# Performance work log

Hardware: AMD Instinct MI355X
Metric: run time of the kernel (lower is better)

## Reference

```python
import jax, jax.numpy as jnp
import numpy as np

N_ATOM, N_QUERY, KNN = 100000, 20000, 32
E = N_QUERY * KNN
HID, EDGE_F, HEADS = 128, 16, 8
D_HEAD = HID // HEADS
LN_EPS = 1e-5


def setup_inputs() -> dict:
    key = jax.random.key(0)
    ks = jax.random.split(key, 16)
    s = 1.0 / np.sqrt(HID)
    src = jax.random.randint(ks[0], (E,), 0, N_ATOM)
    dst = jnp.repeat(jnp.arange(N_QUERY), KNN)  # each query has KNN incoming edges
    return {
        "h_atom": jax.random.normal(ks[1], (N_ATOM, HID), jnp.float32),
        "h_query": jax.random.normal(ks[2], (N_QUERY, HID), jnp.float32),
        "edge_attr": jax.random.uniform(ks[3], (E, EDGE_F), jnp.float32),
        "W_q": jax.random.normal(ks[4], (HID, HID), jnp.float32) * s,
        "W_k": jax.random.normal(ks[5], (HID, HID), jnp.float32) * s,
        "W_v": jax.random.normal(ks[6], (HID, HID), jnp.float32) * s,
        "W_rbf": jax.random.normal(ks[7], (HEADS, EDGE_F), jnp.float32) * (1.0 / np.sqrt(EDGE_F)),
        "W1": jax.random.normal(ks[8], (HID, 2 * HID), jnp.float32) * (1.0 / np.sqrt(2 * HID)),
        "b1": jnp.zeros((HID,), jnp.float32),
        "W2": jax.random.normal(ks[9], (HID, HID), jnp.float32) * s,
        "b2": jnp.zeros((HID,), jnp.float32),
        "ln_gamma": jnp.ones((HID,), jnp.float32),
        "ln_beta": jnp.zeros((HID,), jnp.float32),
        "edge_index": jnp.stack([src, dst]),
        "n_query": N_QUERY,
    }


def reference(h_atom, h_query, edge_attr, W_q, W_k, W_v, W_rbf, W1, b1, W2, b2,
              ln_gamma, ln_beta, edge_index, n_query):
    src, dst = edge_index[0], edge_index[1]
    En = src.shape[0]
    # gather + project, per-edge multi-head Q/K/V  [E, H, d]
    Q = (h_query[dst] @ W_q.T).reshape(En, HEADS, D_HEAD)
    K = (h_atom[src] @ W_k.T).reshape(En, HEADS, D_HEAD)
    V = (h_atom[src] @ W_v.T).reshape(En, HEADS, D_HEAD)
    scores = jnp.einsum("ehd,ehd->eh", Q, K) / np.sqrt(D_HEAD) + edge_attr @ W_rbf.T  # [E,H]
    # segment softmax over edges sharing the same dst query, per head
    seg_max = jax.lax.stop_gradient(jax.ops.segment_max(scores, dst, num_segments=n_query))
    ex = jnp.exp(scores - seg_max[dst])
    denom = jax.ops.segment_sum(ex, dst, num_segments=n_query)
    alpha = ex / (denom[dst] + 1e-16)  # [E,H]
    # weighted scatter-add aggregation
    msgs = (alpha[:, :, None] * V).reshape(En, HID)
    agg = jax.ops.segment_sum(msgs, dst, num_segments=n_query)  # [Nq, HID]
    # update MLP + residual + LayerNorm
    z = jnp.concatenate([h_query, agg], axis=-1)
    delta = jax.nn.relu(z @ W1.T + b1) @ W2.T + b2
    y = h_query + delta
    mu = y.mean(-1, keepdims=True)
    var = y.var(-1, keepdims=True)
    return (y - mu) / jnp.sqrt(var + LN_EPS) * ln_gamma + ln_beta
```

## Files before the change

kernel.cpp:

```cpp
#include <hip/hip_runtime.h>
#include <hip/hip_bf16.h>
#include <math.h>

#define N_ATOM   100000
#define N_QUERY  20000
#define KNN      32
#define EDGES    (N_QUERY * KNN)

typedef __attribute__((ext_vector_type(8))) short  short8;
typedef __attribute__((ext_vector_type(4))) float  floatx4;
typedef __attribute__((ext_vector_type(2))) float  fx2;

static __device__ __forceinline__ unsigned short f2bf_bits(float f) {
  union { __hip_bfloat16 h; unsigned short u; } cv;
  cv.h = __float2bfloat16(f);
  return cv.u;
}
static __device__ __forceinline__ float bflo(unsigned int u) { return __uint_as_float(u << 16); }
static __device__ __forceinline__ float bfhi(unsigned int u) { return __uint_as_float(u & 0xffff0000u); }

__global__ void pack_all_kernel(const float* __restrict__ Wq, const float* __restrict__ Wk,
                                const float* __restrict__ Wv, const float* __restrict__ W1,
                                const float* __restrict__ W2,
                                const float* __restrict__ edge_attr, const float* __restrict__ Wrbf,
                                unsigned short* __restrict__ WKVp, unsigned short* __restrict__ WQp,
                                unsigned short* __restrict__ W1p,  unsigned short* __restrict__ W2p,
                                float* __restrict__ ED) {
  int tid = blockIdx.x * blockDim.x + threadIdx.x;
  if (tid < 98304) {
    const float *Wa, *Wb; int nsplit, Kd, Nd; unsigned short* dst; float scale = 1.0f;
    int t = tid;
    if (t < 32768)      { Wa = Wk; Wb = Wv; nsplit = 128; Kd = 128; Nd = 256; dst = WKVp; }
    else if (t < 49152) { t -= 32768; Wa = Wq; Wb = Wq; nsplit = 128; Kd = 128; Nd = 128; dst = WQp; scale = 0.25f; }
    else if (t < 81920) { t -= 49152; Wa = W1; Wb = W1; nsplit = 128; Kd = 256; Nd = 128; dst = W1p; }
    else                { t -= 81920; Wa = W2; Wb = W2; nsplit = 128; Kd = 128; Nd = 128; dst = W2p; }
    int j    = t & 7;
    int lane = (t >> 3) & 63;
    int t2   = t >> 9;
    int NT   = Nd >> 4;
    int ntile = t2 % NT;
    int ktile = t2 / NT;
    int k = ktile * 32 + (lane >> 4) * 8 + j;
    int n = ntile * 16 + (lane & 15);
    float v = (n < nsplit) ? Wa[(size_t)n * Kd + k] : Wb[(size_t)(n - nsplit) * Kd + k];
    dst[t] = f2bf_bits(v * scale);
  } else {
    int e = tid - 98304;
    if (e >= EDGES) return;
    const float4* ea = (const float4*)(edge_attr + (size_t)e * 16);
    float4 x0 = ea[0], x1 = ea[1], x2 = ea[2], x3 = ea[3];
    float4 r0, r1;
#pragma unroll
    for (int h = 0; h < 8; h++) {
      const float4* wp = (const float4*)(Wrbf + h * 16);
      float4 w0 = wp[0], w1 = wp[1], w2 = wp[2], w3 = wp[3];
      float d = w0.x*x0.x + w0.y*x0.y + w0.z*x0.z + w0.w*x0.w
              + w1.x*x1.x + w1.y*x1.y + w1.z*x1.z + w1.w*x1.w
              + w2.x*x2.x + w2.y*x2.y + w2.z*x2.z + w2.w*x2.w
              + w3.x*x3.x + w3.y*x3.y + w3.z*x3.z + w3.w*x3.w;
      if (h < 4) ((float*)&r0)[h] = d; else ((float*)&r1)[h - 4] = d;
    }
    float4* dst = (float4*)(ED + (size_t)e * 8);
    dst[0] = r0; dst[1] = r1;
  }
}

__global__ __launch_bounds__(256, 2) void gemm_kvq(
    const float* __restrict__ h_atom, const float* __restrict__ h_query,
    const unsigned short* __restrict__ WKVp, const unsigned short* __restrict__ WQp,
    unsigned char* __restrict__ Kp8, unsigned char* __restrict__ Vp8,
    unsigned short* __restrict__ Qb) {
  constexpr int KB = (N_ATOM + 63) / 64;
  __shared__ unsigned short Wlds[32768];
  const int tid  = threadIdx.x;
  const int l    = tid & 63;
  const int w    = tid >> 6;
  const int quad = l >> 4;
  const int col0 = l & 15;

  if ((int)blockIdx.x < KB) {
    const int row0 = blockIdx.x * 64 + w * 16;
    const int grow = row0 + col0;
    int arow = grow < N_ATOM ? grow : N_ATOM - 1;

    const float* aptr = h_atom + (size_t)arow * 128 + quad * 8;
    floatx4 a[8];
#pragma unroll
    for (int k0 = 0; k0 < 4; k0++) {
      a[2 * k0]     = *(const floatx4*)(aptr + k0 * 32);
      a[2 * k0 + 1] = *(const floatx4*)(aptr + k0 * 32 + 4);
    }

    {
      const uint4* gsrc = (const uint4*)WKVp;
      uint4* ldst = (uint4*)Wlds;
#pragma unroll
      for (int it = 0; it < 16; it++)
        ldst[it * 256 + tid] = gsrc[it * 256 + tid];
    }

    short8 af[4];
#pragma unroll
    for (int k0 = 0; k0 < 4; k0++) {
      af[k0][0] = (short)f2bf_bits(a[2*k0][0]); af[k0][1] = (short)f2bf_bits(a[2*k0][1]);
      af[k0][2] = (short)f2bf_bits(a[2*k0][2]); af[k0][3] = (short)f2bf_bits(a[2*k0][3]);
      af[k0][4] = (short)f2bf_bits(a[2*k0+1][0]); af[k0][5] = (short)f2bf_bits(a[2*k0+1][1]);
      af[k0][6] = (short)f2bf_bits(a[2*k0+1][2]); af[k0][7] = (short)f2bf_bits(a[2*k0+1][3]);
    }
    __syncthreads();

    floatx4 acc[16];
#pragma unroll
    for (int i = 0; i < 16; i++) acc[i] = (floatx4){0.f, 0.f, 0.f, 0.f};
#pragma unroll
    for (int k0 = 0; k0 < 4; k0++) {
      const unsigned short* bbase = Wlds + k0 * 16 * 512 + l * 8;
#pragma unroll
      for (int nt = 0; nt < 16; nt++) {
        short8 bf = *(const short8*)(bbase + nt * 512);
        acc[nt] = __builtin_amdgcn_mfma_f32_16x16x32_bf16(bf, af[k0], acc[nt], 0, 0, 0);
      }
    }

    if (grow < N_ATOM) {
      unsigned char* kbase = Kp8 + (size_t)grow * 128 + quad * 4;
      unsigned char* vbase = Vp8 + (size_t)grow * 128 + quad * 4;
#pragma unroll
      for (int nt = 0; nt < 16; nt++) {
        int pk = __builtin_amdgcn_cvt_pk_fp8_f32(acc[nt][0], acc[nt][1], 0, false);
        pk     = __builtin_amdgcn_cvt_pk_fp8_f32(acc[nt][2], acc[nt][3], pk, true);
        if (nt < 8) *(int*)(kbase + nt * 16) = pk;
        else        *(int*)(vbase + (nt - 8) * 16) = pk;
      }
    }
  } else {
    const int row0 = ((int)blockIdx.x - KB) * 64 + w * 16;
    const int grow = row0 + col0;
    int arow = grow < N_QUERY ? grow : N_QUERY - 1;

    const float* aptr = h_query + (size_t)arow * 128 + quad * 8;
    floatx4 a[8];
#pragma unroll
    for (int k0 = 0; k0 < 4; k0++) {
      a[2 * k0]     = *(const floatx4*)(aptr + k0 * 32);
      a[2 * k0 + 1] = *(const floatx4*)(aptr + k0 * 32 + 4);
    }
    {
      const uint4* gsrc = (const uint4*)WQp;
      uint4* ldst = (uint4*)Wlds;
#pragma unroll
      for (int it = 0; it < 8; it++)
        ldst[it * 256 + tid] = gsrc[it * 256 + tid];
    }
    short8 af[4];
#pragma unroll
    for (int k0 = 0; k0 < 4; k0++) {
      af[k0][0] = (short)f2bf_bits(a[2*k0][0]); af[k0][1] = (short)f2bf_bits(a[2*k0][1]);
      af[k0][2] = (short)f2bf_bits(a[2*k0][2]); af[k0][3] = (short)f2bf_bits(a[2*k0][3]);
      af[k0][4] = (short)f2bf_bits(a[2*k0+1][0]); af[k0][5] = (short)f2bf_bits(a[2*k0+1][1]);
      af[k0][6] = (short)f2bf_bits(a[2*k0+1][2]); af[k0][7] = (short)f2bf_bits(a[2*k0+1][3]);
    }
    __syncthreads();

    floatx4 acc[8];
#pragma unroll
    for (int i = 0; i < 8; i++) acc[i] = (floatx4){0.f, 0.f, 0.f, 0.f};
#pragma unroll
    for (int k0 = 0; k0 < 4; k0++) {
      const unsigned short* bbase = Wlds + k0 * 8 * 512 + l * 8;
#pragma unroll
      for (int nt = 0; nt < 8; nt++) {
        short8 bf = *(const short8*)(bbase + nt * 512);
        acc[nt] = __builtin_amdgcn_mfma_f32_16x16x32_bf16(bf, af[k0], acc[nt], 0, 0, 0);
      }
    }

    if (grow < N_QUERY) {
#pragma unroll
      for (int nt = 0; nt < 8; nt++) {
        unsigned u0 = (unsigned)f2bf_bits(acc[nt][0]) | ((unsigned)f2bf_bits(acc[nt][1]) << 16);
        unsigned u1 = (unsigned)f2bf_bits(acc[nt][2]) | ((unsigned)f2bf_bits(acc[nt][3]) << 16);
        uint2 uu; uu.x = u0; uu.y = u1;
        *(uint2*)(Qb + (size_t)grow * 128 + nt * 16 + quad * 4) = uu;
      }
    }
  }
}

__global__ __launch_bounds__(256, 4) void attn_kernel(
    const unsigned short* __restrict__ Qb,
    const unsigned char* __restrict__ Kp8,
    const unsigned char* __restrict__ Vp8,
    const float* __restrict__ ED,
    const int* __restrict__ src,
    float* __restrict__ Agg) {
  const int l = threadIdx.x & 63;
  const int w = threadIdx.x >> 6;
  const int q = blockIdx.x * 4 + w;
  const int j = l >> 3;
  const int h = l & 7;
  const int e0 = q * KNN;

  int s0 = src[e0 +  0 + j];
  int s1 = src[e0 +  8 + j];
  int s2 = src[e0 + 16 + j];
  int s3 = src[e0 + 24 + j];

  const float* edp = ED + (size_t)e0 * 8 + l;
  float ed0 = edp[0];
  float ed1 = edp[64];
  float ed2 = edp[128];
  float ed3 = edp[192];

  const uint4* qp = (const uint4*)(Qb + (size_t)q * 128 + h * 16);
  uint4 qA = qp[0], qB = qp[1];

  uint4 kq0 = *(const uint4*)(Kp8 + (size_t)s0 * 128 + h * 16);
  uint4 kq1 = *(const uint4*)(Kp8 + (size_t)s1 * 128 + h * 16);
  uint4 kq2 = *(const uint4*)(Kp8 + (size_t)s2 * 128 + h * 16);
  uint4 kq3 = *(const uint4*)(Kp8 + (size_t)s3 * 128 + h * 16);
  uint4 vq0 = *(const uint4*)(Vp8 + (size_t)s0 * 128 + h * 16);
  uint4 vq1 = *(const uint4*)(Vp8 + (size_t)s1 * 128 + h * 16);
  uint4 vq2 = *(const uint4*)(Vp8 + (size_t)s2 * 128 + h * 16);
  uint4 vq3 = *(const uint4*)(Vp8 + (size_t)s3 * 128 + h * 16);

  float qd[16];
  qd[0]  = bflo(qA.x); qd[1]  = bfhi(qA.x); qd[2]  = bflo(qA.y); qd[3]  = bfhi(qA.y);
  qd[4]  = bflo(qA.z); qd[5]  = bfhi(qA.z); qd[6]  = bflo(qA.w); qd[7]  = bfhi(qA.w);
  qd[8]  = bflo(qB.x); qd[9]  = bfhi(qB.x); qd[10] = bflo(qB.y); qd[11] = bfhi(qB.y);
  qd[12] = bflo(qB.z); qd[13] = bfhi(qB.z); qd[14] = bflo(qB.w); qd[15] = bfhi(qB.w);

  float acc[16];
#pragma unroll
  for (int i = 0; i < 16; i++) acc[i] = 0.f;
  float lsum = 0.f;

  auto dopass = [&](const uint4& kq, const uint4& vq, float ed) {
    float kd = 0.f;
    {
      fx2 f0, f1;
      f0 = __builtin_amdgcn_cvt_pk_f32_fp8((int)kq.x, false);
      f1 = __builtin_amdgcn_cvt_pk_f32_fp8((int)kq.x, true);
      kd += qd[0] * f0[0] + qd[1] * f0[1] + qd[2] * f1[0] + qd[3] * f1[1];
      f0 = __builtin_amdgcn_cvt_pk_f32_fp8((int)kq.y, false);
      f1 = __builtin_amdgcn_cvt_pk_f32_fp8((int)kq.y, true);
      kd += qd[4] * f0[0] + qd[5] * f0[1] + qd[6] * f1[0] + qd[7] * f1[1];
      f0 = __builtin_amdgcn_cvt_pk_f32_fp8((int)kq.z, false);
      f1 = __builtin_amdgcn_cvt_pk_f32_fp8((int)kq.z, true);
      kd += qd[8] * f0[0] + qd[9] * f0[1] + qd[10] * f1[0] + qd[11] * f1[1];
      f0 = __builtin_amdgcn_cvt_pk_f32_fp8((int)kq.w, false);
      f1 = __builtin_amdgcn_cvt_pk_f32_fp8((int)kq.w, true);
      kd += qd[12] * f0[0] + qd[13] * f0[1] + qd[14] * f1[0] + qd[15] * f1[1];
    }
    float pe = __expf(kd + ed);
    lsum += pe;
    {
      fx2 g0, g1;
      g0 = __builtin_amdgcn_cvt_pk_f32_fp8((int)vq.x, false);
      g1 = __builtin_amdgcn_cvt_pk_f32_fp8((int)vq.x, true);
      acc[0] += pe * g0[0]; acc[1] += pe * g0[1]; acc[2] += pe * g1[0]; acc[3] += pe * g1[1];
      g0 = __builtin_amdgcn_cvt_pk_f32_fp8((int)vq.y, false);
      g1 = __builtin_amdgcn_cvt_pk_f32_fp8((int)vq.y, true);
      acc[4] += pe * g0[0]; acc[5] += pe * g0[1]; acc[6] += pe * g1[0]; acc[7] += pe * g1[1];
      g0 = __builtin_amdgcn_cvt_pk_f32_fp8((int)vq.z, false);
      g1 = __builtin_amdgcn_cvt_pk_f32_fp8((int)vq.z, true);
      acc[8] += pe * g0[0]; acc[9] += pe * g0[1]; acc[10] += pe * g1[0]; acc[11] += pe * g1[1];
      g0 = __builtin_amdgcn_cvt_pk_f32_fp8((int)vq.w, false);
      g1 = __builtin_amdgcn_cvt_pk_f32_fp8((int)vq.w, true);
      acc[12] += pe * g0[0]; acc[13] += pe * g0[1]; acc[14] += pe * g1[0]; acc[15] += pe * g1[1];
    }
  };
  dopass(kq0, vq0, ed0);
  dopass(kq1, vq1, ed1);
  dopass(kq2, vq2, ed2);
  dopass(kq3, vq3, ed3);

  lsum += __shfl_xor(lsum, 8, 64);
  lsum += __shfl_xor(lsum, 16, 64);
  lsum += __shfl_xor(lsum, 32, 64);

  float r8[8];
  const bool hiA = (l & 32) != 0;
#pragma unroll
  for (int i = 0; i < 8; i++) {
    float keep = hiA ? acc[i + 8] : acc[i];
    float send = hiA ? acc[i]     : acc[i + 8];
    r8[i] = keep + __shfl_xor(send, 32, 64);
  }
  float r4[4];
  const bool hiB = (l & 16) != 0;
#pragma unroll
  for (int i = 0; i < 4; i++) {
    float keep = hiB ? r8[i + 4] : r8[i];
    float send = hiB ? r8[i]     : r8[i + 4];
    r4[i] = keep + __shfl_xor(send, 16, 64);
  }
  float r2[2];
  const bool hiC = (l & 8) != 0;
#pragma unroll
  for (int i = 0; i < 2; i++) {
    float keep = hiC ? r4[i + 2] : r4[i];
    float send = hiC ? r4[i]     : r4[i + 2];
    r2[i] = keep + __shfl_xor(send, 8, 64);
  }
  float inv = 1.f / (lsum + 1e-16f);
  float2 o; o.x = r2[0] * inv; o.y = r2[1] * inv;
  *(float2*)(Agg + (size_t)q * 128 + h * 16 + 2 * j) = o;
}

__global__ __launch_bounds__(256, 1) void mlp_kernel(
    const float* __restrict__ h_query, const float* __restrict__ Agg,
    const unsigned short* __restrict__ W1p, const unsigned short* __restrict__ W2p,
    const float* __restrict__ b1, const float* __restrict__ b2,
    const float* __restrict__ gamma, const float* __restrict__ beta,
    float* __restrict__ out) {
  constexpr int M = N_QUERY;
  constexpr int STRIDE = 136;
  __shared__ unsigned short Wlds[16384];
  __shared__ unsigned short hid[64 * STRIDE];

  const int tid  = threadIdx.x;
  const int l    = tid & 63;
  const int w    = tid >> 6;
  const int quad = l >> 4;
  const int col0 = l & 15;
  const int row0 = blockIdx.x * 64 + w * 16;
  const int grow = row0 + col0;
  const int arow = grow < M ? grow : M - 1;

  const float* hp = h_query + (size_t)arow * 128 + quad * 8;
  const float* gp = Agg     + (size_t)arow * 128 + quad * 8;
  floatx4 a[16];
#pragma unroll
  for (int k0 = 0; k0 < 4; k0++) {
    a[2*k0]       = *(const floatx4*)(hp + k0 * 32);
    a[2*k0+1]     = *(const floatx4*)(hp + k0 * 32 + 4);
    a[8 + 2*k0]   = *(const floatx4*)(gp + k0 * 32);
    a[8 + 2*k0+1] = *(const floatx4*)(gp + k0 * 32 + 4);
  }

  {
    const uint4* gsrc = (const uint4*)W1p;
    uint4* ldst = (uint4*)Wlds;
#pragma unroll
    for (int it = 0; it < 8; it++) ldst[it * 256 + tid] = gsrc[it * 256 + tid];
  }

  short8 af[8];
#pragma unroll
  for (int t = 0; t < 8; t++) {
    af[t][0] = (short)f2bf_bits(a[2*t][0]);   af[t][1] = (short)f2bf_bits(a[2*t][1]);
    af[t][2] = (short)f2bf_bits(a[2*t][2]);   af[t][3] = (short)f2bf_bits(a[2*t][3]);
    af[t][4] = (short)f2bf_bits(a[2*t+1][0]); af[t][5] = (short)f2bf_bits(a[2*t+1][1]);
    af[t][6] = (short)f2bf_bits(a[2*t+1][2]); af[t][7] = (short)f2bf_bits(a[2*t+1][3]);
  }
  __syncthreads();

  floatx4 acc[8];
#pragma unroll
  for (int i = 0; i < 8; i++) acc[i] = (floatx4){0.f, 0.f, 0.f, 0.f};
#pragma unroll
  for (int kt = 0; kt < 4; kt++) {
    const unsigned short* bbase = Wlds + kt * 4096 + l * 8;
#pragma unroll
    for (int nt = 0; nt < 8; nt++) {
      short8 bf = *(const short8*)(bbase + nt * 512);
      acc[nt] = __builtin_amdgcn_mfma_f32_16x16x32_bf16(bf, af[kt], acc[nt], 0, 0, 0);
    }
  }
  __syncthreads();

  {
    const uint4* gsrc = (const uint4*)(W1p + 16384);
    uint4* ldst = (uint4*)Wlds;
#pragma unroll
    for (int it = 0; it < 8; it++) ldst[it * 256 + tid] = gsrc[it * 256 + tid];
  }
  __syncthreads();

#pragma unroll
  for (int kt = 0; kt < 4; kt++) {
    const unsigned short* bbase = Wlds + kt * 4096 + l * 8;
#pragma unroll
    for (int nt = 0; nt < 8; nt++) {
      short8 bf = *(const short8*)(bbase + nt * 512);
      acc[nt] = __builtin_amdgcn_mfma_f32_16x16x32_bf16(bf, af[4 + kt], acc[nt], 0, 0, 0);
    }
  }

  {
    const int rl = w * 16 + col0;
#pragma unroll
    for (int nt = 0; nt < 8; nt++) {
      const int c = nt * 16 + quad * 4;
      float4 bb = *(const float4*)(b1 + c);
      unsigned u0 = (unsigned)f2bf_bits(fmaxf(acc[nt][0] + bb.x, 0.f))
                  | ((unsigned)f2bf_bits(fmaxf(acc[nt][1] + bb.y, 0.f)) << 16);
      unsigned u1 = (unsigned)f2bf_bits(fmaxf(acc[nt][2] + bb.z, 0.f))
                  | ((unsigned)f2bf_bits(fmaxf(acc[nt][3] + bb.w, 0.f)) << 16);
      uint2 uu; uu.x = u0; uu.y = u1;
      *(uint2*)(hid + rl * STRIDE + c) = uu;
    }
  }
  __syncthreads();

  {
    const uint4* gsrc = (const uint4*)W2p;
    uint4* ldst = (uint4*)Wlds;
#pragma unroll
    for (int it = 0; it < 8; it++) ldst[it * 256 + tid] = gsrc[it * 256 + tid];
  }
  __syncthreads();

  floatx4 acc2[8];
#pragma unroll
  for (int i = 0; i < 8; i++) acc2[i] = (floatx4){0.f, 0.f, 0.f, 0.f};
  const int rloc = w * 16 + col0;
#pragma unroll
  for (int k0 = 0; k0 < 128; k0 += 32) {
    short8 af2 = *(const short8*)(hid + rloc * STRIDE + k0 + quad * 8);
    const unsigned short* bbase = Wlds + (k0 >> 5) * 4096 + l * 8;
#pragma unroll
    for (int nt = 0; nt < 8; nt++) {
      short8 bf = *(const short8*)(bbase + nt * 512);
      acc2[nt] = __builtin_amdgcn_mfma_f32_16x16x32_bf16(bf, af2, acc2[nt], 0, 0, 0);
    }
  }

  const int rr = grow < M ? grow : M - 1;
  float v[8][4];
  float s1 = 0.f, s2 = 0.f;
#pragma unroll
  for (int nt = 0; nt < 8; nt++) {
    const int c = nt * 16 + quad * 4;
    float4 hq = *(const float4*)(h_query + (size_t)rr * 128 + c);
    float4 bb = *(const float4*)(b2 + c);
    float t0 = acc2[nt][0] + bb.x + hq.x;
    float t1 = acc2[nt][1] + bb.y + hq.y;
    float t2 = acc2[nt][2] + bb.z + hq.z;
    float t3 = acc2[nt][3] + bb.w + hq.w;
    v[nt][0] = t0; v[nt][1] = t1; v[nt][2] = t2; v[nt][3] = t3;
    s1 += t0 + t1 + t2 + t3;
    s2 += t0 * t0 + t1 * t1 + t2 * t2 + t3 * t3;
  }
  s1 += __shfl_xor(s1, 16, 64); s1 += __shfl_xor(s1, 32, 64);
  s2 += __shfl_xor(s2, 16, 64); s2 += __shfl_xor(s2, 32, 64);
  float mean = s1 * (1.0f / 128.0f);
  float var  = s2 * (1.0f / 128.0f) - mean * mean;
  float rstd = rsqrtf(var + 1e-5f);
  if (grow < M) {
#pragma unroll
    for (int nt = 0; nt < 8; nt++) {
      const int c = nt * 16 + quad * 4;
      float4 gg = *(const float4*)(gamma + c);
      float4 be = *(const float4*)(beta + c);
      float4 o;
      o.x = (v[nt][0] - mean) * rstd * gg.x + be.x;
      o.y = (v[nt][1] - mean) * rstd * gg.y + be.y;
      o.z = (v[nt][2] - mean) * rstd * gg.z + be.z;
      o.w = (v[nt][3] - mean) * rstd * gg.w + be.w;
      *(float4*)(out + (size_t)grow * 128 + c) = o;
    }
  }
}

extern "C" void kernel_launch(void* const* d_in, const int* in_sizes, int n_in,
                              void* d_out, int out_size, void* d_ws, size_t ws_size,
                              hipStream_t stream) {
  const float* h_atom    = (const float*)d_in[0];
  const float* h_query   = (const float*)d_in[1];
  const float* edge_attr = (const float*)d_in[2];
  const float* W_q  = (const float*)d_in[3];
  const float* W_k  = (const float*)d_in[4];
  const float* W_v  = (const float*)d_in[5];
  const float* Wrbf = (const float*)d_in[6];
  const float* W1   = (const float*)d_in[7];
  const float* b1   = (const float*)d_in[8];
  const float* W2   = (const float*)d_in[9];
  const float* b2   = (const float*)d_in[10];
  const float* ln_g = (const float*)d_in[11];
  const float* ln_b = (const float*)d_in[12];
  const int* edge_index = (const int*)d_in[13];
  float* out = (float*)d_out;

  char* ws = (char*)d_ws;
  unsigned char*  Kp8 = (unsigned char*)(ws);
  unsigned char*  Vp8 = (unsigned char*)(ws + 12800000);
  unsigned short* Qb  = (unsigned short*)(ws + 25600000);
  float* Agg          = (float*)(ws + 30720000);
  unsigned short* WKVp = (unsigned short*)(ws + 40960000);
  unsigned short* WQp  = WKVp + 32768;
  unsigned short* W1p  = WQp  + 16384;
  unsigned short* W2p  = W1p  + 32768;
  float* ED           = (float*)(ws + 41160704);

  pack_all_kernel<<<(98304 + EDGES + 255) / 256, 256, 0, stream>>>(
      W_q, W_k, W_v, W1, W2, edge_attr, Wrbf, WKVp, WQp, W1p, W2p, ED);

  constexpr int KB = (N_ATOM + 63) / 64;
  constexpr int QB = (N_QUERY + 63) / 64;
  gemm_kvq<<<KB + QB, 256, 0, stream>>>(h_atom, h_query, WKVp, WQp, Kp8, Vp8, Qb);

  attn_kernel<<<N_QUERY / 4, 256, 0, stream>>>(Qb, Kp8, Vp8, ED, edge_index, Agg);

  mlp_kernel<<<(N_QUERY + 63) / 64, 256, 0, stream>>>(
      h_query, Agg, W1p, W2p, b1, b2, ln_g, ln_b, out);
}
```

Before: 210.3 us.

## Make KV/Q projection GEMM persistent with register-prefetched input rows

```diff
diff --git a/kernel.cpp b/kernel.cpp
--- a/kernel.cpp
+++ b/kernel.cpp
@@ -70,119 +70,163 @@
     const unsigned short* __restrict__ WKVp, const unsigned short* __restrict__ WQp,
     unsigned char* __restrict__ Kp8, unsigned char* __restrict__ Vp8,
     unsigned short* __restrict__ Qb) {
-  constexpr int KB = (N_ATOM + 63) / 64;
+  constexpr int KVGROUPS = (N_ATOM + 63) / 64;
+  constexpr int QGROUPS  = (N_QUERY + 63) / 64;
+  constexpr int KVB = 464;
   __shared__ unsigned short Wlds[32768];
   const int tid  = threadIdx.x;
   const int l    = tid & 63;
   const int w    = tid >> 6;
   const int quad = l >> 4;
   const int col0 = l & 15;
-
-  if ((int)blockIdx.x < KB) {
-    const int row0 = blockIdx.x * 64 + w * 16;
-    const int grow = row0 + col0;
-    int arow = grow < N_ATOM ? grow : N_ATOM - 1;
-
-    const float* aptr = h_atom + (size_t)arow * 128 + quad * 8;
+  const int woff = w * 16 + col0;
+  const bool isKV = (int)blockIdx.x < KVB;
+
+  if (isKV) {
+    const uint4* gsrc = (const uint4*)WKVp;
+    uint4* ldst = (uint4*)Wlds;
+#pragma unroll
+    for (int it = 0; it < 16; it++) ldst[it * 256 + tid] = gsrc[it * 256 + tid];
+  } else {
+    const uint4* gsrc = (const uint4*)WQp;
+    uint4* ldst = (uint4*)Wlds;
+#pragma unroll
+    for (int it = 0; it < 8; it++) ldst[it * 256 + tid] = gsrc[it * 256 + tid];
+  }
+
+  if (isKV) {
+    int g = (int)blockIdx.x;
     floatx4 a[8];
-#pragma unroll
-    for (int k0 = 0; k0 < 4; k0++) {
-      a[2 * k0]     = *(const floatx4*)(aptr + k0 * 32);
-      a[2 * k0 + 1] = *(const floatx4*)(aptr + k0 * 32 + 4);
-    }
-
     {
-      const uint4* gsrc = (const uint4*)WKVp;
-      uint4* ldst = (uint4*)Wlds;
-#pragma unroll
-      for (int it = 0; it < 16; it++)
-        ldst[it * 256 + tid] = gsrc[it * 256 + tid];
-    }
-
-    short8 af[4];
-#pragma unroll
-    for (int k0 = 0; k0 < 4; k0++) {
-      af[k0][0] = (short)f2bf_bits(a[2*k0][0]); af[k0][1] = (short)f2bf_bits(a[2*k0][1]);
-      af[k0][2] = (short)f2bf_bits(a[2*k0][2]); af[k0][3] = (short)f2bf_bits(a[2*k0][3]);
-      af[k0][4] = (short)f2bf_bits(a[2*k0+1][0]); af[k0][5] = (short)f2bf_bits(a[2*k0+1][1]);
-      af[k0][6] = (short)f2bf_bits(a[2*k0+1][2]); af[k0][7] = (short)f2bf_bits(a[2*k0+1][3]);
+      int r = g * 64 + woff; if (r >= N_ATOM) r = N_ATOM - 1;
+      const float* ap = h_atom + (size_t)r * 128 + quad * 8;
+#pragma unroll
+      for (int k0 = 0; k0 < 4; k0++) {
+        a[2*k0]   = *(const floatx4*)(ap + k0 * 32);
+        a[2*k0+1] = *(const floatx4*)(ap + k0 * 32 + 4);
+      }
     }
     __syncthreads();
 
-    floatx4 acc[16];
-#pragma unroll
-    for (int i = 0; i < 16; i++) acc[i] = (floatx4){0.f, 0.f, 0.f, 0.f};
-#pragma unroll
-    for (int k0 = 0; k0 < 4; k0++) {
-      const unsigned short* bbase = Wlds + k0 * 16 * 512 + l * 8;
-#pragma unroll
-      for (int nt = 0; nt < 16; nt++) {
-        short8 bf = *(const short8*)(bbase + nt * 512);
-        acc[nt] = __builtin_amdgcn_mfma_f32_16x16x32_bf16(bf, af[k0], acc[nt], 0, 0, 0);
-      }
-    }
-
-    if (grow < N_ATOM) {
-      unsigned char* kbase = Kp8 + (size_t)grow * 128 + quad * 4;
-      unsigned char* vbase = Vp8 + (size_t)grow * 128 + quad * 4;
-#pragma unroll
-      for (int nt = 0; nt < 16; nt++) {
-        int pk = __builtin_amdgcn_cvt_pk_fp8_f32(acc[nt][0], acc[nt][1], 0, false);
-        pk     = __builtin_amdgcn_cvt_pk_fp8_f32(acc[nt][2], acc[nt][3], pk, true);
-        if (nt < 8) *(int*)(kbase + nt * 16) = pk;
-        else        *(int*)(vbase + (nt - 8) * 16) = pk;
-      }
+    for (; g < KVGROUPS; g += KVB) {
+      const int gn = g + KVB;
+      floatx4 an[8];
+#pragma unroll
+      for (int i = 0; i < 8; i++) an[i] = (floatx4){0.f, 0.f, 0.f, 0.f};
+      if (gn < KVGROUPS) {
+        int r = gn * 64 + woff; if (r >= N_ATOM) r = N_ATOM - 1;
+        const float* ap = h_atom + (size_t)r * 128 + quad * 8;
+#pragma unroll
+        for (int k0 = 0; k0 < 4; k0++) {
+          an[2*k0]   = *(const floatx4*)(ap + k0 * 32);
+          an[2*k0+1] = *(const floatx4*)(ap + k0 * 32 + 4);
+        }
+      }
+      __builtin_amdgcn_sched_barrier(0);
+
+      short8 af[4];
+#pragma unroll
+      for (int k0 = 0; k0 < 4; k0++) {
+        af[k0][0] = (short)f2bf_bits(a[2*k0][0]);   af[k0][1] = (short)f2bf_bits(a[2*k0][1]);
+        af[k0][2] = (short)f2bf_bits(a[2*k0][2]);   af[k0][3] = (short)f2bf_bits(a[2*k0][3]);
+        af[k0][4] = (short)f2bf_bits(a[2*k0+1][0]); af[k0][5] = (short)f2bf_bits(a[2*k0+1][1]);
+        af[k0][6] = (short)f2bf_bits(a[2*k0+1][2]); af[k0][7] = (short)f2bf_bits(a[2*k0+1][3]);
+      }
+
+      floatx4 acc[16];
+#pragma unroll
+      for (int i = 0; i < 16; i++) acc[i] = (floatx4){0.f, 0.f, 0.f, 0.f};
+#pragma unroll
+      for (int k0 = 0; k0 < 4; k0++) {
+        const unsigned short* bbase = Wlds + k0 * 8192 + l * 8;
+#pragma unroll
+        for (int nt = 0; nt < 16; nt++) {
+          short8 bf = *(const short8*)(bbase + nt * 512);
+          acc[nt] = __builtin_amdgcn_mfma_f32_16x16x32_bf16(bf, af[k0], acc[nt], 0, 0, 0);
+        }
+      }
+
+      const int grow = g * 64 + woff;
+      if (grow < N_ATOM) {
+        unsigned char* kbase = Kp8 + (size_t)grow * 128 + quad * 4;
+        unsigned char* vbase = Vp8 + (size_t)grow * 128 + quad * 4;
+#pragma unroll
+        for (int nt = 0; nt < 16; nt++) {
+          int pk = __builtin_amdgcn_cvt_pk_fp8_f32(acc[nt][0], acc[nt][1], 0, false);
+          pk     = __builtin_amdgcn_cvt_pk_fp8_f32(acc[nt][2], acc[nt][3], pk, true);
+          if (nt < 8) *(int*)(kbase + nt * 16) = pk;
+          else        *(int*)(vbase + (nt - 8) * 16) = pk;
+        }
+      }
+
+#pragma unroll
+      for (int i = 0; i < 8; i++) a[i] = an[i];
     }
   } else {
-    const int row0 = ((int)blockIdx.x - KB) * 64 + w * 16;
-    const int grow = row0 + col0;
-    int arow = grow < N_QUERY ? grow : N_QUERY - 1;
-
-    const float* aptr = h_query + (size_t)arow * 128 + quad * 8;
+    int g = (int)blockIdx.x - KVB;
     floatx4 a[8];
-#pragma unroll
-    for (int k0 = 0; k0 < 4; k0++) {
-      a[2 * k0]     = *(const floatx4*)(aptr + k0 * 32);
-      a[2 * k0 + 1] = *(const floatx4*)(aptr + k0 * 32 + 4);
-    }
     {
-      const uint4* gsrc = (const uint4*)WQp;
-      uint4* ldst = (uint4*)Wlds;
-#pragma unroll
-      for (int it = 0; it < 8; it++)
-        ldst[it * 256 + tid] = gsrc[it * 256 + tid];
-    }
-    short8 af[4];
-#pragma unroll
-    for (int k0 = 0; k0 < 4; k0++) {
-      af[k0][0] = (short)f2bf_bits(a[2*k0][0]); af[k0][1] = (short)f2bf_bits(a[2*k0][1]);
-      af[k0][2] = (short)f2bf_bits(a[2*k0][2]); af[k0][3] = (short)f2bf_bits(a[2*k0][3]);
-      af[k0][4] = (short)f2bf_bits(a[2*k0+1][0]); af[k0][5] = (short)f2bf_bits(a[2*k0+1][1]);
-      af[k0][6] = (short)f2bf_bits(a[2*k0+1][2]); af[k0][7] = (short)f2bf_bits(a[2*k0+1][3]);
+      int r = g * 64 + woff; if (r >= N_QUERY) r = N_QUERY - 1;
+      const float* ap = h_query + (size_t)r * 128 + quad * 8;
+#pragma unroll
+      for (int k0 = 0; k0 < 4; k0++) {
+        a[2*k0]   = *(const floatx4*)(ap + k0 * 32);
+        a[2*k0+1] = *(const floatx4*)(ap + k0 * 32 + 4);
+      }
     }
     __syncthreads();
 
-    floatx4 acc[8];
-#pragma unroll
-    for (int i = 0; i < 8; i++) acc[i] = (floatx4){0.f, 0.f, 0.f, 0.f};
-#pragma unroll
-    for (int k0 = 0; k0 < 4; k0++) {
-      const unsigned short* bbase = Wlds + k0 * 8 * 512 + l * 8;
-#pragma unroll
-      for (int nt = 0; nt < 8; nt++) {
-        short8 bf = *(const short8*)(bbase + nt * 512);
-        acc[nt] = __builtin_amdgcn_mfma_f32_16x16x32_bf16(bf, af[k0], acc[nt], 0, 0, 0);
-      }
-    }
-
-    if (grow < N_QUERY) {
-#pragma unroll
-      for (int nt = 0; nt < 8; nt++) {
-        unsigned u0 = (unsigned)f2bf_bits(acc[nt][0]) | ((unsigned)f2bf_bits(acc[nt][1]) << 16);
-        unsigned u1 = (unsigned)f2bf_bits(acc[nt][2]) | ((unsigned)f2bf_bits(acc[nt][3]) << 16);
-        uint2 uu; uu.x = u0; uu.y = u1;
-        *(uint2*)(Qb + (size_t)grow * 128 + nt * 16 + quad * 4) = uu;
-      }
+    for (; g < QGROUPS; g += 512 - KVB) {
+      const int gn = g + (512 - KVB);
+      floatx4 an[8];
+#pragma unroll
+      for (int i = 0; i < 8; i++) an[i] = (floatx4){0.f, 0.f, 0.f, 0.f};
+      if (gn < QGROUPS) {
+        int r = gn * 64 + woff; if (r >= N_QUERY) r = N_QUERY - 1;
+        const float* ap = h_query + (size_t)r * 128 + quad * 8;
+#pragma unroll
+        for (int k0 = 0; k0 < 4; k0++) {
+          an[2*k0]   = *(const floatx4*)(ap + k0 * 32);
+          an[2*k0+1] = *(const floatx4*)(ap + k0 * 32 + 4);
+        }
+      }
+      __builtin_amdgcn_sched_barrier(0);
+
+      short8 af[4];
+#pragma unroll
+      for (int k0 = 0; k0 < 4; k0++) {
+        af[k0][0] = (short)f2bf_bits(a[2*k0][0]);   af[k0][1] = (short)f2bf_bits(a[2*k0][1]);
+        af[k0][2] = (short)f2bf_bits(a[2*k0][2]);   af[k0][3] = (short)f2bf_bits(a[2*k0][3]);
+        af[k0][4] = (short)f2bf_bits(a[2*k0+1][0]); af[k0][5] = (short)f2bf_bits(a[2*k0+1][1]);
+        af[k0][6] = (short)f2bf_bits(a[2*k0+1][2]); af[k0][7] = (short)f2bf_bits(a[2*k0+1][3]);
+      }
+
+      floatx4 acc[8];
+#pragma unroll
+      for (int i = 0; i < 8; i++) acc[i] = (floatx4){0.f, 0.f, 0.f, 0.f};
+#pragma unroll
+      for (int k0 = 0; k0 < 4; k0++) {
+        const unsigned short* bbase = Wlds + k0 * 4096 + l * 8;
+#pragma unroll
+        for (int nt = 0; nt < 8; nt++) {
+          short8 bf = *(const short8*)(bbase + nt * 512);
+          acc[nt] = __builtin_amdgcn_mfma_f32_16x16x32_bf16(bf, af[k0], acc[nt], 0, 0, 0);
+        }
+      }
+
+      const int grow = g * 64 + woff;
+      if (grow < N_QUERY) {
+#pragma unroll
+        for (int nt = 0; nt < 8; nt++) {
+          unsigned u0 = (unsigned)f2bf_bits(acc[nt][0]) | ((unsigned)f2bf_bits(acc[nt][1]) << 16);
+          unsigned u1 = (unsigned)f2bf_bits(acc[nt][2]) | ((unsigned)f2bf_bits(acc[nt][3]) << 16);
+          uint2 uu; uu.x = u0; uu.y = u1;
+          *(uint2*)(Qb + (size_t)grow * 128 + nt * 16 + quad * 4) = uu;
+        }
+      }
+
+#pragma unroll
+      for (int i = 0; i < 8; i++) a[i] = an[i];
     }
   }
 }
@@ -497,9 +541,7 @@
   pack_all_kernel<<<(98304 + EDGES + 255) / 256, 256, 0, stream>>>(
       W_q, W_k, W_v, W1, W2, edge_attr, Wrbf, WKVp, WQp, W1p, W2p, ED);
 
-  constexpr int KB = (N_ATOM + 63) / 64;
-  constexpr int QB = (N_QUERY + 63) / 64;
-  gemm_kvq<<<KB + QB, 256, 0, stream>>>(h_atom, h_query, WKVp, WQp, Kp8, Vp8, Qb);
+  gemm_kvq<<<512, 256, 0, stream>>>(h_atom, h_query, WKVp, WQp, Kp8, Vp8, Qb);
 
   attn_kernel<<<N_QUERY / 4, 256, 0, stream>>>(Qb, Kp8, Vp8, ED, edge_index, Agg);
 
```

After: 214.5 us. 2.0% more time.

## Fold edge RBF projection into GEMM launch and store aggregation as bf16

Applied to the files above, without the earlier changes.

```diff
diff --git a/kernel.cpp b/kernel.cpp
--- a/kernel.cpp
+++ b/kernel.cpp
@@ -22,64 +22,47 @@
 __global__ void pack_all_kernel(const float* __restrict__ Wq, const float* __restrict__ Wk,
                                 const float* __restrict__ Wv, const float* __restrict__ W1,
                                 const float* __restrict__ W2,
-                                const float* __restrict__ edge_attr, const float* __restrict__ Wrbf,
                                 unsigned short* __restrict__ WKVp, unsigned short* __restrict__ WQp,
-                                unsigned short* __restrict__ W1p,  unsigned short* __restrict__ W2p,
-                                float* __restrict__ ED) {
+                                unsigned short* __restrict__ W1p,  unsigned short* __restrict__ W2p) {
   int tid = blockIdx.x * blockDim.x + threadIdx.x;
-  if (tid < 98304) {
-    const float *Wa, *Wb; int nsplit, Kd, Nd; unsigned short* dst; float scale = 1.0f;
-    int t = tid;
-    if (t < 32768)      { Wa = Wk; Wb = Wv; nsplit = 128; Kd = 128; Nd = 256; dst = WKVp; }
-    else if (t < 49152) { t -= 32768; Wa = Wq; Wb = Wq; nsplit = 128; Kd = 128; Nd = 128; dst = WQp; scale = 0.25f; }
-    else if (t < 81920) { t -= 49152; Wa = W1; Wb = W1; nsplit = 128; Kd = 256; Nd = 128; dst = W1p; }
-    else                { t -= 81920; Wa = W2; Wb = W2; nsplit = 128; Kd = 128; Nd = 128; dst = W2p; }
-    int j    = t & 7;
-    int lane = (t >> 3) & 63;
-    int t2   = t >> 9;
-    int NT   = Nd >> 4;
-    int ntile = t2 % NT;
-    int ktile = t2 / NT;
-    int k = ktile * 32 + (lane >> 4) * 8 + j;
-    int n = ntile * 16 + (lane & 15);
-    float v = (n < nsplit) ? Wa[(size_t)n * Kd + k] : Wb[(size_t)(n - nsplit) * Kd + k];
-    dst[t] = f2bf_bits(v * scale);
-  } else {
-    int e = tid - 98304;
-    if (e >= EDGES) return;
-    const float4* ea = (const float4*)(edge_attr + (size_t)e * 16);
-    float4 x0 = ea[0], x1 = ea[1], x2 = ea[2], x3 = ea[3];
-    float4 r0, r1;
-#pragma unroll
-    for (int h = 0; h < 8; h++) {
-      const float4* wp = (const float4*)(Wrbf + h * 16);
-      float4 w0 = wp[0], w1 = wp[1], w2 = wp[2], w3 = wp[3];
-      float d = w0.x*x0.x + w0.y*x0.y + w0.z*x0.z + w0.w*x0.w
-              + w1.x*x1.x + w1.y*x1.y + w1.z*x1.z + w1.w*x1.w
-              + w2.x*x2.x + w2.y*x2.y + w2.z*x2.z + w2.w*x2.w
-              + w3.x*x3.x + w3.y*x3.y + w3.z*x3.z + w3.w*x3.w;
-      if (h < 4) ((float*)&r0)[h] = d; else ((float*)&r1)[h - 4] = d;
-    }
-    float4* dst = (float4*)(ED + (size_t)e * 8);
-    dst[0] = r0; dst[1] = r1;
-  }
+  if (tid >= 98304) return;
+  const float *Wa, *Wb; int nsplit, Kd, Nd; unsigned short* dst; float scale = 1.0f;
+  int t = tid;
+  if (t < 32768)      { Wa = Wk; Wb = Wv; nsplit = 128; Kd = 128; Nd = 256; dst = WKVp; }
+  else if (t < 49152) { t -= 32768; Wa = Wq; Wb = Wq; nsplit = 128; Kd = 128; Nd = 128; dst = WQp; scale = 0.25f; }
+  else if (t < 81920) { t -= 49152; Wa = W1; Wb = W1; nsplit = 128; Kd = 256; Nd = 128; dst = W1p; }
+  else                { t -= 81920; Wa = W2; Wb = W2; nsplit = 128; Kd = 128; Nd = 128; dst = W2p; }
+  int j    = t & 7;
+  int lane = (t >> 3) & 63;
+  int t2   = t >> 9;
+  int NT   = Nd >> 4;
+  int ntile = t2 % NT;
+  int ktile = t2 / NT;
+  int k = ktile * 32 + (lane >> 4) * 8 + j;
+  int n = ntile * 16 + (lane & 15);
+  float v = (n < nsplit) ? Wa[(size_t)n * Kd + k] : Wb[(size_t)(n - nsplit) * Kd + k];
+  dst[t] = f2bf_bits(v * scale);
 }
 
 __global__ __launch_bounds__(256, 2) void gemm_kvq(
     const float* __restrict__ h_atom, const float* __restrict__ h_query,
     const unsigned short* __restrict__ WKVp, const unsigned short* __restrict__ WQp,
+    const float* __restrict__ edge_attr, const float* __restrict__ Wrbf,
     unsigned char* __restrict__ Kp8, unsigned char* __restrict__ Vp8,
-    unsigned short* __restrict__ Qb) {
-  constexpr int KB = (N_ATOM + 63) / 64;
+    unsigned short* __restrict__ Qb, float* __restrict__ ED) {
+  constexpr int KB  = (N_ATOM + 63) / 64;
+  constexpr int QB  = (N_QUERY + 63) / 64;
+  constexpr int EDB = 1280;
   __shared__ unsigned short Wlds[32768];
   const int tid  = threadIdx.x;
   const int l    = tid & 63;
   const int w    = tid >> 6;
   const int quad = l >> 4;
   const int col0 = l & 15;
-
-  if ((int)blockIdx.x < KB) {
-    const int row0 = blockIdx.x * 64 + w * 16;
+  const int bid  = (int)blockIdx.x;
+
+  if (bid < KB) {
+    const int row0 = bid * 64 + w * 16;
     const int grow = row0 + col0;
     int arow = grow < N_ATOM ? grow : N_ATOM - 1;
 
@@ -90,7 +73,6 @@
       a[2 * k0]     = *(const floatx4*)(aptr + k0 * 32);
       a[2 * k0 + 1] = *(const floatx4*)(aptr + k0 * 32 + 4);
     }
-
     {
       const uint4* gsrc = (const uint4*)WKVp;
       uint4* ldst = (uint4*)Wlds;
@@ -98,7 +80,6 @@
       for (int it = 0; it < 16; it++)
         ldst[it * 256 + tid] = gsrc[it * 256 + tid];
     }
-
     short8 af[4];
 #pragma unroll
     for (int k0 = 0; k0 < 4; k0++) {
@@ -121,7 +102,6 @@
         acc[nt] = __builtin_amdgcn_mfma_f32_16x16x32_bf16(bf, af[k0], acc[nt], 0, 0, 0);
       }
     }
-
     if (grow < N_ATOM) {
       unsigned char* kbase = Kp8 + (size_t)grow * 128 + quad * 4;
       unsigned char* vbase = Vp8 + (size_t)grow * 128 + quad * 4;
@@ -133,8 +113,8 @@
         else        *(int*)(vbase + (nt - 8) * 16) = pk;
       }
     }
-  } else {
-    const int row0 = ((int)blockIdx.x - KB) * 64 + w * 16;
+  } else if (bid < KB + QB) {
+    const int row0 = (bid - KB) * 64 + w * 16;
     const int grow = row0 + col0;
     int arow = grow < N_QUERY ? grow : N_QUERY - 1;
 
@@ -174,7 +154,6 @@
         acc[nt] = __builtin_amdgcn_mfma_f32_16x16x32_bf16(bf, af[k0], acc[nt], 0, 0, 0);
       }
     }
-
     if (grow < N_QUERY) {
 #pragma unroll
       for (int nt = 0; nt < 8; nt++) {
@@ -184,6 +163,28 @@
         *(uint2*)(Qb + (size_t)grow * 128 + nt * 16 + quad * 4) = uu;
       }
     }
+  } else {
+    int e = (bid - (KB + QB)) * 256 + tid;
+#pragma unroll
+    for (int it = 0; it < 2; it++, e += EDB * 256) {
+      if (e < EDGES) {
+        const float4* ea = (const float4*)(edge_attr + (size_t)e * 16);
+        float4 x0 = ea[0], x1 = ea[1], x2 = ea[2], x3 = ea[3];
+        float4 r0, r1;
+#pragma unroll
+        for (int h = 0; h < 8; h++) {
+          const float4* wp = (const float4*)(Wrbf + h * 16);
+          float4 w0 = wp[0], w1 = wp[1], w2 = wp[2], w3 = wp[3];
+          float d = w0.x*x0.x + w0.y*x0.y + w0.z*x0.z + w0.w*x0.w
+                  + w1.x*x1.x + w1.y*x1.y + w1.z*x1.z + w1.w*x1.w
+                  + w2.x*x2.x + w2.y*x2.y + w2.z*x2.z + w2.w*x2.w
+                  + w3.x*x3.x + w3.y*x3.y + w3.z*x3.z + w3.w*x3.w;
+          if (h < 4) ((float*)&r0)[h] = d; else ((float*)&r1)[h - 4] = d;
+        }
+        float4* dst = (float4*)(ED + (size_t)e * 8);
+        dst[0] = r0; dst[1] = r1;
+      }
+    }
   }
 }
 
@@ -193,7 +194,7 @@
     const unsigned char* __restrict__ Vp8,
     const float* __restrict__ ED,
     const int* __restrict__ src,
-    float* __restrict__ Agg) {
+    unsigned short* __restrict__ Agg16) {
   const int l = threadIdx.x & 63;
   const int w = threadIdx.x >> 6;
   const int q = blockIdx.x * 4 + w;
@@ -304,12 +305,12 @@
     r2[i] = keep + __shfl_xor(send, 8, 64);
   }
   float inv = 1.f / (lsum + 1e-16f);
-  float2 o; o.x = r2[0] * inv; o.y = r2[1] * inv;
-  *(float2*)(Agg + (size_t)q * 128 + h * 16 + 2 * j) = o;
+  unsigned o16 = (unsigned)f2bf_bits(r2[0] * inv) | ((unsigned)f2bf_bits(r2[1] * inv) << 16);
+  *(unsigned*)(Agg16 + (size_t)q * 128 + h * 16 + 2 * j) = o16;
 }
 
 __global__ __launch_bounds__(256, 1) void mlp_kernel(
-    const float* __restrict__ h_query, const float* __restrict__ Agg,
+    const float* __restrict__ h_query, const unsigned short* __restrict__ Agg16,
     const unsigned short* __restrict__ W1p, const unsigned short* __restrict__ W2p,
     const float* __restrict__ b1, const float* __restrict__ b2,
     const float* __restrict__ gamma, const float* __restrict__ beta,
@@ -329,14 +330,14 @@
   const int arow = grow < M ? grow : M - 1;
 
   const float* hp = h_query + (size_t)arow * 128 + quad * 8;
-  const float* gp = Agg     + (size_t)arow * 128 + quad * 8;
-  floatx4 a[16];
+  const unsigned short* gp = Agg16 + (size_t)arow * 128;
+  floatx4 a[8];
+  short8 afg[4];
 #pragma unroll
   for (int k0 = 0; k0 < 4; k0++) {
-    a[2*k0]       = *(const floatx4*)(hp + k0 * 32);
-    a[2*k0+1]     = *(const floatx4*)(hp + k0 * 32 + 4);
-    a[8 + 2*k0]   = *(const floatx4*)(gp + k0 * 32);
-    a[8 + 2*k0+1] = *(const floatx4*)(gp + k0 * 32 + 4);
+    a[2*k0]   = *(const floatx4*)(hp + k0 * 32);
+    a[2*k0+1] = *(const floatx4*)(hp + k0 * 32 + 4);
+    afg[k0]   = *(const short8*)(gp + k0 * 32 + quad * 8);
   }
 
   {
@@ -346,9 +347,9 @@
     for (int it = 0; it < 8; it++) ldst[it * 256 + tid] = gsrc[it * 256 + tid];
   }
 
-  short8 af[8];
-#pragma unroll
-  for (int t = 0; t < 8; t++) {
+  short8 af[4];
+#pragma unroll
+  for (int t = 0; t < 4; t++) {
     af[t][0] = (short)f2bf_bits(a[2*t][0]);   af[t][1] = (short)f2bf_bits(a[2*t][1]);
     af[t][2] = (short)f2bf_bits(a[2*t][2]);   af[t][3] = (short)f2bf_bits(a[2*t][3]);
     af[t][4] = (short)f2bf_bits(a[2*t+1][0]); af[t][5] = (short)f2bf_bits(a[2*t+1][1]);
@@ -384,7 +385,7 @@
 #pragma unroll
     for (int nt = 0; nt < 8; nt++) {
       short8 bf = *(const short8*)(bbase + nt * 512);
-      acc[nt] = __builtin_amdgcn_mfma_f32_16x16x32_bf16(bf, af[4 + kt], acc[nt], 0, 0, 0);
+      acc[nt] = __builtin_amdgcn_mfma_f32_16x16x32_bf16(bf, afg[kt], acc[nt], 0, 0, 0);
     }
   }
 
@@ -484,25 +485,27 @@
   float* out = (float*)d_out;
 
   char* ws = (char*)d_ws;
-  unsigned char*  Kp8 = (unsigned char*)(ws);
-  unsigned char*  Vp8 = (unsigned char*)(ws + 12800000);
-  unsigned short* Qb  = (unsigned short*)(ws + 25600000);
-  float* Agg          = (float*)(ws + 30720000);
+  unsigned char*  Kp8  = (unsigned char*)(ws);
+  unsigned char*  Vp8  = (unsigned char*)(ws + 12800000);
+  unsigned short* Qb   = (unsigned short*)(ws + 25600000);
+  unsigned short* Agg16= (unsigned short*)(ws + 30720000);
   unsigned short* WKVp = (unsigned short*)(ws + 40960000);
   unsigned short* WQp  = WKVp + 32768;
   unsigned short* W1p  = WQp  + 16384;
   unsigned short* W2p  = W1p  + 32768;
-  float* ED           = (float*)(ws + 41160704);
-
-  pack_all_kernel<<<(98304 + EDGES + 255) / 256, 256, 0, stream>>>(
-      W_q, W_k, W_v, W1, W2, edge_attr, Wrbf, WKVp, WQp, W1p, W2p, ED);
-
-  constexpr int KB = (N_ATOM + 63) / 64;
-  constexpr int QB = (N_QUERY + 63) / 64;
-  gemm_kvq<<<KB + QB, 256, 0, stream>>>(h_atom, h_query, WKVp, WQp, Kp8, Vp8, Qb);
-
-  attn_kernel<<<N_QUERY / 4, 256, 0, stream>>>(Qb, Kp8, Vp8, ED, edge_index, Agg);
+  float* ED            = (float*)(ws + 41160704);
+
+  pack_all_kernel<<<(98304 + 255) / 256, 256, 0, stream>>>(
+      W_q, W_k, W_v, W1, W2, WKVp, WQp, W1p, W2p);
+
+  constexpr int KB  = (N_ATOM + 63) / 64;
+  constexpr int QB  = (N_QUERY + 63) / 64;
+  constexpr int EDB = 1280;
+  gemm_kvq<<<KB + QB + EDB, 256, 0, stream>>>(
+      h_atom, h_query, WKVp, WQp, edge_attr, Wrbf, Kp8, Vp8, Qb, ED);
+
+  attn_kernel<<<N_QUERY / 4, 256, 0, stream>>>(Qb, Kp8, Vp8, ED, edge_index, Agg16);
 
   mlp_kernel<<<(N_QUERY + 63) / 64, 256, 0, stream>>>(
-      h_query, Agg, W1p, W2p, b1, b2, ln_g, ln_b, out);
+      h_query, Agg16, W1p, W2p, b1, b2, ln_g, ln_b, out);
 }
```

New measurement: 205.2 us. 1.02x faster.
